# Kernel optimization log

Hardware: AMD Instinct MI355X
Metric: run time of the kernel (lower is better)

## Reference

```python
import jax, jax.numpy as jnp
import numpy as np

C = 512
C8 = C // 8  # 64
B, L = 32, 1024


def setup_inputs() -> dict:
    key = jax.random.key(0)
    ks = jax.random.split(key, 8)
    s = 0.05
    return {
        "x": jax.random.normal(ks[0], (B, C, L), dtype=jnp.float32),
        "Wq": jax.random.normal(ks[1], (C8, C), dtype=jnp.float32) * s,
        "bq": jax.random.normal(ks[2], (C8,), dtype=jnp.float32) * s,
        "Wk": jax.random.normal(ks[3], (C8, C), dtype=jnp.float32) * s,
        "bk": jax.random.normal(ks[4], (C8,), dtype=jnp.float32) * s,
        "Wv": jax.random.normal(ks[5], (C, C), dtype=jnp.float32) * s,
        "bv": jax.random.normal(ks[6], (C,), dtype=jnp.float32) * s,
        "gamma": jax.random.normal(ks[7], (1,), dtype=jnp.float32) * s,
    }


def reference(x, Wq, bq, Wk, bk, Wv, bv, gamma):
    # kernel-size-1 Conv1d == per-position matmul over channels
    q = jnp.einsum('dc,bcl->bdl', Wq, x) + bq[None, :, None]  # [B, C8, L]
    k = jnp.einsum('dc,bcl->bdl', Wk, x) + bk[None, :, None]  # [B, C8, L]
    v = jnp.einsum('oc,bcl->bol', Wv, x) + bv[None, :, None]  # [B, C, L]
    # energy[b, l, m] = <q[:, l], k[:, m]>  (no 1/sqrt(d) scaling, as in source)
    energy = jnp.einsum('bdl,bdm->blm', q, k)                 # [B, L, L]
    attention = jax.nn.softmax(energy, axis=-1)               # softmax over m
    # out[b, c, l] = sum_m v[b, c, m] * attention[b, l, m]
    out = jnp.einsum('bcm,blm->bcl', v, attention)            # [B, C, L]
    out = gamma[0] * out + x
    return (out, attention)
```

## Files before the change

kernel.cpp:

```cpp
#include <hip/hip_runtime.h>

typedef __attribute__((ext_vector_type(8))) short short8;
typedef __attribute__((ext_vector_type(4))) float f32x4;

#define B_SZ 32
#define C_IN 512
#define C8V 64
#define LSEQ 1024
#define OUT_ELEMS (B_SZ * C_IN * LSEQ)

__device__ inline unsigned short bf16_rn(float f) {
  unsigned int u = __float_as_uint(f);
  unsigned int r = 0x7FFFu + ((u >> 16) & 1u);
  return (unsigned short)((u + r) >> 16);
}
__device__ inline float bf16_to_f32(unsigned short h) {
  return __uint_as_float(((unsigned int)h) << 16);
}
__device__ inline void split_bf16(float f, unsigned short &hi, unsigned short &lo) {
  hi = bf16_rn(f);
  lo = bf16_rn(f - bf16_to_f32(hi));
}

__global__ __launch_bounds__(256) void split_weights(
    const float* __restrict__ Wq, const float* __restrict__ Wk, const float* __restrict__ Wv,
    unsigned short* __restrict__ Wqh, unsigned short* __restrict__ Wql,
    unsigned short* __restrict__ Wkh, unsigned short* __restrict__ Wkl,
    unsigned short* __restrict__ Wvh)
{
  int i = (blockIdx.x * 256 + threadIdx.x) * 4;
  if (i < 262144) {
    f32x4 f = *(const f32x4*)&Wv[i];
    #pragma unroll
    for (int j = 0; j < 4; ++j) Wvh[i + j] = bf16_rn(f[j]);
  } else if (i < 294912) {
    int k = i - 262144;
    f32x4 f = *(const f32x4*)&Wq[k];
    #pragma unroll
    for (int j = 0; j < 4; ++j) { unsigned short h, l; split_bf16(f[j], h, l); Wqh[k+j] = h; Wql[k+j] = l; }
  } else {
    int k = i - 294912;
    f32x4 f = *(const f32x4*)&Wk[k];
    #pragma unroll
    for (int j = 0; j < 4; ++j) { unsigned short h, l; split_bf16(f[j], h, l); Wkh[k+j] = h; Wkl[k+j] = l; }
  }
}

__global__ __launch_bounds__(256, 2) void qk_proj(
    const float* __restrict__ x,
    const unsigned short* __restrict__ Wqh, const unsigned short* __restrict__ Wql,
    const unsigned short* __restrict__ Wkh, const unsigned short* __restrict__ Wkl,
    const float* __restrict__ bq, const float* __restrict__ bk,
    unsigned short* __restrict__ qh, unsigned short* __restrict__ ql,
    unsigned short* __restrict__ kh, unsigned short* __restrict__ kl)
{
  const int nt = blockIdx.x;
  const int b  = blockIdx.y;
  const int tid = threadIdx.x;
  const int wave = tid >> 6, lane = tid & 63;
  const int wr = wave >> 1, wc = wave & 1;
  const int g = lane >> 4, ln = lane & 15;

  __shared__ char smem[66560];
  unsigned short* Ah = (unsigned short*)smem;
  unsigned short* Al = Ah + 128*64;
  unsigned short* Bh = Al + 128*64;
  unsigned short* Bl = Bh + 64*64;
  float* xs = (float*)(Bl + 64*64);

  f32x4 acc[4][2] = {};

  for (int kb = 0; kb < 8; ++kb) {
    if (kb) __syncthreads();
    #pragma unroll
    for (int i = 0; i < 4; ++i) {
      int idx = tid + i*256;
      int r = idx >> 3, jj = idx & 7;
      const unsigned short* sH = (r < 64) ? &Wqh[r*512 + kb*64 + jj*8]
                                          : &Wkh[(r-64)*512 + kb*64 + jj*8];
      const unsigned short* sL = (r < 64) ? &Wql[r*512 + kb*64 + jj*8]
                                          : &Wkl[(r-64)*512 + kb*64 + jj*8];
      int dst = r*64 + ((jj ^ (r & 7)) << 3);
      *(short8*)&Ah[dst] = *(const short8*)sH;
      *(short8*)&Al[dst] = *(const short8*)sL;
    }
    #pragma unroll
    for (int i = 0; i < 4; ++i) {
      int idx = tid + i*256;
      int kk = idx >> 4, l4 = idx & 15;
      f32x4 v = *(const f32x4*)&x[((long)b*C_IN + kb*64 + kk)*LSEQ + nt*64 + l4*4];
      *(f32x4*)&xs[kk*68 + l4*4] = v;
    }
    __syncthreads();
    {
      int l = tid & 63, kc = (tid >> 6) * 16;
      unsigned short hbuf[16], lbuf[16];
      #pragma unroll
      for (int i = 0; i < 16; ++i) split_bf16(xs[(kc + i)*68 + l], hbuf[i], lbuf[i]);
      #pragma unroll
      for (int s2 = 0; s2 < 2; ++s2) {
        int s = (kc >> 3) + s2;
        int dst = l*64 + ((s ^ (l & 7)) << 3);
        *(short8*)&Bh[dst] = *(const short8*)&hbuf[s2*8];
        *(short8*)&Bl[dst] = *(const short8*)&lbuf[s2*8];
      }
    }
    __syncthreads();
    __builtin_amdgcn_s_setprio(1);
    #pragma unroll
    for (int ks = 0; ks < 2; ++ks) {
      short8 bhf[2], blf[2];
      #pragma unroll
      for (int ni = 0; ni < 2; ++ni) {
        int cr = wc*32 + ni*16 + ln;
        int s = ((ks*4 + g) ^ (cr & 7)) << 3;
        bhf[ni] = *(const short8*)&Bh[cr*64 + s];
        blf[ni] = *(const short8*)&Bl[cr*64 + s];
      }
      #pragma unroll
      for (int mi = 0; mi < 4; ++mi) {
        int ar = wr*64 + mi*16 + ln;
        int s = ((ks*4 + g) ^ (ar & 7)) << 3;
        short8 ahf = *(const short8*)&Ah[ar*64 + s];
        short8 alf = *(const short8*)&Al[ar*64 + s];
        #pragma unroll
        for (int ni = 0; ni < 2; ++ni) {
          acc[mi][ni] = __builtin_amdgcn_mfma_f32_16x16x32_bf16(ahf, bhf[ni], acc[mi][ni], 0,0,0);
          acc[mi][ni] = __builtin_amdgcn_mfma_f32_16x16x32_bf16(ahf, blf[ni], acc[mi][ni], 0,0,0);
          acc[mi][ni] = __builtin_amdgcn_mfma_f32_16x16x32_bf16(alf, bhf[ni], acc[mi][ni], 0,0,0);
        }
      }
    }
    __builtin_amdgcn_s_setprio(0);
  }
  __syncthreads();
  unsigned short* Trh = (unsigned short*)smem;
  unsigned short* Trl = Trh + 64*136;
  #pragma unroll
  for (int mi = 0; mi < 4; ++mi)
    #pragma unroll
    for (int ni = 0; ni < 2; ++ni)
      #pragma unroll
      for (int j = 0; j < 4; ++j) {
        int rloc = wr*64 + mi*16 + g*4 + j;
        int cloc = wc*32 + ni*16 + ln;
        float bias = (rloc < 64) ? bq[rloc] : bk[rloc - 64];
        unsigned short hi, lo; split_bf16(acc[mi][ni][j] + bias, hi, lo);
        Trh[cloc*136 + rloc] = hi;
        Trl[cloc*136 + rloc] = lo;
      }
  __syncthreads();
  #pragma unroll
  for (int i = 0; i < 4; ++i) {
    int idx = tid + i*256;
    int l = idx >> 4, s = idx & 15;
    long row = ((long)b*LSEQ + nt*64 + l) * 64;
    short8 h  = *(const short8*)&Trh[l*136 + s*8];
    short8 lo = *(const short8*)&Trl[l*136 + s*8];
    if (s < 8) { *(short8*)&qh[row + s*8] = h;      *(short8*)&ql[row + s*8] = lo; }
    else       { *(short8*)&kh[row + (s-8)*8] = h;  *(short8*)&kl[row + (s-8)*8] = lo; }
  }
}

__global__ __launch_bounds__(256, 2) void v_proj(
    const float* __restrict__ x,
    const unsigned short* __restrict__ Wvh,
    const float* __restrict__ bv,
    unsigned short* __restrict__ vws)
{
  const int gi = blockIdx.x;
  const int b  = (gi & 7) + 8 * (gi >> 8);
  const int t  = (gi >> 3) & 31;
  const int lt = t & 7, ct = t >> 3;
  const int tid = threadIdx.x;
  const int wave = tid >> 6, lane = tid & 63;
  const int wr = wave >> 1, wc = wave & 1;
  const int g = lane >> 4, ln = lane & 15;

  __shared__ char smem[66560];
  unsigned short* Ahs = (unsigned short*)smem;
  unsigned short* Bhs = Ahs + 8192;
  float* xs = (float*)(Bhs + 8192);

  f32x4 acc[4][4] = {};

  for (int kb = 0; kb < 8; ++kb) {
    if (kb) __syncthreads();
    #pragma unroll
    for (int i = 0; i < 4; ++i) {
      int idx = tid + i*256;
      int r = idx >> 3, jj = idx & 7;
      *(short8*)&Ahs[r*64 + ((jj ^ (r & 7)) << 3)] =
        *(const short8*)&Wvh[(ct*128 + r)*512 + kb*64 + jj*8];
    }
    #pragma unroll
    for (int i = 0; i < 8; ++i) {
      int idx = tid + i*256;
      int kk = idx >> 5, l4 = idx & 31;
      f32x4 v = *(const f32x4*)&x[((long)b*C_IN + kb*64 + kk)*LSEQ + lt*128 + l4*4];
      *(f32x4*)&xs[kk*132 + l4*4] = v;
    }
    __syncthreads();
    {
      int l = tid & 127, kc = (tid >> 7) * 32;
      unsigned short hbuf[32];
      #pragma unroll
      for (int i = 0; i < 32; ++i) hbuf[i] = bf16_rn(xs[(kc + i)*132 + l]);
      #pragma unroll
      for (int s2 = 0; s2 < 4; ++s2) {
        int s = (kc >> 3) + s2;
        *(short8*)&Bhs[l*64 + ((s ^ (l & 7)) << 3)] = *(const short8*)&hbuf[s2*8];
      }
    }
    __syncthreads();
    __builtin_amdgcn_s_setprio(1);
    #pragma unroll
    for (int ks = 0; ks < 2; ++ks) {
      short8 bf[4];
      #pragma unroll
      for (int ni = 0; ni < 4; ++ni) {
        int cr = wc*64 + ni*16 + ln;
        bf[ni] = *(const short8*)&Bhs[cr*64 + (((ks*4 + g) ^ (cr & 7)) << 3)];
      }
      #pragma unroll
      for (int mi = 0; mi < 4; ++mi) {
        int ar = wr*64 + mi*16 + ln;
        short8 af = *(const short8*)&Ahs[ar*64 + (((ks*4 + g) ^ (ar & 7)) << 3)];
        #pragma unroll
        for (int ni = 0; ni < 4; ++ni)
          acc[mi][ni] = __builtin_amdgcn_mfma_f32_16x16x32_bf16(af, bf[ni], acc[mi][ni], 0,0,0);
      }
    }
    __builtin_amdgcn_s_setprio(0);
  }
  __syncthreads();
  unsigned short* Tr = (unsigned short*)smem;
  #pragma unroll
  for (int mi = 0; mi < 4; ++mi)
    #pragma unroll
    for (int ni = 0; ni < 4; ++ni)
      #pragma unroll
      for (int j = 0; j < 4; ++j) {
        int rloc = wr*64 + mi*16 + g*4 + j;
        int cloc = wc*64 + ni*16 + ln;
        Tr[rloc*136 + cloc] = bf16_rn(acc[mi][ni][j] + bv[ct*128 + rloc]);
      }
  __syncthreads();
  #pragma unroll
  for (int i = 0; i < 8; ++i) {
    int idx = tid + i*256;
    int c = idx >> 4, s = idx & 15;
    *(short8*)&vws[((long)b*C_IN + ct*128 + c)*LSEQ + lt*128 + s*8] =
      *(const short8*)&Tr[c*136 + s*8];
  }
}

__global__ __launch_bounds__(256, 2) void energy_softmax(
    const unsigned short* __restrict__ qh, const unsigned short* __restrict__ ql,
    const unsigned short* __restrict__ kh, const unsigned short* __restrict__ kl,
    float* __restrict__ attn, unsigned short* __restrict__ pbuf)
{
  const int gi = blockIdx.x;
  const int b  = (gi & 7) + 8 * (gi >> 9);
  const int lt = (gi >> 3) & 63;
  const int tid = threadIdx.x;
  const int wave = tid >> 6, lane = tid & 63;
  const int g = lane >> 4, ln = lane & 15;

  __shared__ unsigned short Ksm[16640];
  __shared__ float redM[4][16];
  __shared__ float redS[4][16];
  unsigned short* Kh = Ksm;
  unsigned short* Kl = Ksm + 8192;

  short8 ah[2], al[2];
  {
    long qrow = ((long)b*LSEQ + lt*16 + ln) * 64;
    #pragma unroll
    for (int ks = 0; ks < 2; ++ks) {
      ah[ks] = *(const short8*)&qh[qrow + ks*32 + g*8];
      al[ks] = *(const short8*)&ql[qrow + ks*32 + g*8];
    }
  }

  const int rb = tid >> 3, jj = tid & 7;
  const int dst0 = rb*64 + ((jj ^ (rb & 7)) << 3);
  const long kbase = ((long)b*LSEQ + rb)*64 + jj*8;

  short8 rkh[4], rkl[4];
  #pragma unroll
  for (int j = 0; j < 4; ++j) {
    rkh[j] = *(const short8*)&kh[kbase + j*2048];
    rkl[j] = *(const short8*)&kl[kbase + j*2048];
  }

  f32x4 acc[8][2] = {};
  #pragma unroll
  for (int c = 0; c < 8; ++c) {
    __syncthreads();
    #pragma unroll
    for (int j = 0; j < 4; ++j) {
      *(short8*)&Kh[dst0 + j*2048] = rkh[j];
      *(short8*)&Kl[dst0 + j*2048] = rkl[j];
    }
    __syncthreads();
    if (c < 7) {
      #pragma unroll
      for (int j = 0; j < 4; ++j) {
        rkh[j] = *(const short8*)&kh[kbase + (long)(c+1)*8192 + j*2048];
        rkl[j] = *(const short8*)&kl[kbase + (long)(c+1)*8192 + j*2048];
      }
    }
    __builtin_amdgcn_s_setprio(1);
    #pragma unroll
    for (int fq = 0; fq < 2; ++fq) {
      int mloc = wave*32 + fq*16 + ln;
      #pragma unroll
      for (int ks = 0; ks < 2; ++ks) {
        int s = ((ks*4 + g) ^ (mloc & 7)) << 3;
        short8 bh = *(const short8*)&Kh[mloc*64 + s];
        short8 bl = *(const short8*)&Kl[mloc*64 + s];
        acc[c][fq] = __builtin_amdgcn_mfma_f32_16x16x32_bf16(ah[ks], bh, acc[c][fq], 0,0,0);
        acc[c][fq] = __builtin_amdgcn_mfma_f32_16x16x32_bf16(ah[ks], bl, acc[c][fq], 0,0,0);
        acc[c][fq] = __builtin_amdgcn_mfma_f32_16x16x32_bf16(al[ks], bh, acc[c][fq], 0,0,0);
      }
    }
    __builtin_amdgcn_s_setprio(0);
  }

  float mx[4];
  #pragma unroll
  for (int j = 0; j < 4; ++j) {
    float m = -1e30f;
    #pragma unroll
    for (int c = 0; c < 8; ++c)
      #pragma unroll
      for (int fq = 0; fq < 2; ++fq) m = fmaxf(m, acc[c][fq][j]);
    #pragma unroll
    for (int off = 1; off < 16; off <<= 1) m = fmaxf(m, __shfl_xor(m, off));
    mx[j] = m;
  }
  if (ln == 0) {
    #pragma unroll
    for (int j = 0; j < 4; ++j) redM[wave][g*4+j] = mx[j];
  }
  __syncthreads();
  #pragma unroll
  for (int j = 0; j < 4; ++j) {
    float m = redM[0][g*4+j];
    #pragma unroll
    for (int w = 1; w < 4; ++w) m = fmaxf(m, redM[w][g*4+j]);
    mx[j] = m;
  }
  float sm[4];
  #pragma unroll
  for (int j = 0; j < 4; ++j) {
    float s = 0.f;
    #pragma unroll
    for (int c = 0; c < 8; ++c)
      #pragma unroll
      for (int fq = 0; fq < 2; ++fq) {
        float p = __expf(acc[c][fq][j] - mx[j]);
        acc[c][fq][j] = p;
        s += p;
      }
    #pragma unroll
    for (int off = 1; off < 16; off <<= 1) s += __shfl_xor(s, off);
    sm[j] = s;
  }
  if (ln == 0) {
    #pragma unroll
    for (int j = 0; j < 4; ++j) redS[wave][g*4+j] = sm[j];
  }
  __syncthreads();
  #pragma unroll
  for (int j = 0; j < 4; ++j) {
    float s = redS[0][g*4+j];
    #pragma unroll
    for (int w = 1; w < 4; ++w) s += redS[w][g*4+j];
    sm[j] = 1.0f / s;
  }

  unsigned short* Pb = Ksm;
  __syncthreads();
  #pragma unroll
  for (int c = 0; c < 8; ++c)
    #pragma unroll
    for (int fq = 0; fq < 2; ++fq) {
      int m0 = c*128 + wave*32 + fq*16 + ln;
      #pragma unroll
      for (int j = 0; j < 4; ++j)
        Pb[(g*4+j)*1032 + m0] = bf16_rn(acc[c][fq][j] * sm[j]);
    }
  __syncthreads();
  #pragma unroll
  for (int u = 0; u < 8; ++u) {
    int cid = tid + u*256;
    int row = cid >> 7, col = (cid & 127) * 8;
    short8 v = *(const short8*)&Pb[row*1032 + col];
    long gro = ((long)b*LSEQ + lt*16 + row)*LSEQ + col;
    *(short8*)&pbuf[gro] = v;
    f32x4 f0, f1;
    #pragma unroll
    for (int i = 0; i < 4; ++i) {
      f0[i] = bf16_to_f32((unsigned short)v[i]);
      f1[i] = bf16_to_f32((unsigned short)v[i+4]);
    }
    *(f32x4*)&attn[gro] = f0;
    *(f32x4*)&attn[gro + 4] = f1;
  }
}

__global__ __launch_bounds__(512, 2) void pv_out(
    const unsigned short* __restrict__ vws,
    const unsigned short* __restrict__ pbuf,
    const float* __restrict__ x,
    const float* __restrict__ gamma,
    float* __restrict__ out)
{
  const int gi = blockIdx.x;
  const int b  = (gi & 7) + 8 * (gi >> 7);
  const int t  = (gi >> 3) & 15;
  const int lt = t >> 2, ct = t & 3;
  const int tid = threadIdx.x;
  const int w = tid >> 6, lane = tid & 63;
  const int wcq = w >> 2, wlq = w & 3;
  const int g = lane >> 4, ln = lane & 15;

  __shared__ char smem[49152];
  unsigned short* Vst = (unsigned short*)smem;
  unsigned short* Pst = (unsigned short*)(smem + 16384);

  const int vr = tid >> 2, vs0 = (tid & 3) * 2;
  const long vbase = ((long)b*C_IN + ct*128 + vr)*LSEQ + vs0*8;
  const int pr = tid >> 1, ps0 = (tid & 1) * 4;
  const long pbase = ((long)b*LSEQ + lt*256 + pr)*LSEQ + ps0*8;

  f32x4 acc[4][4] = {};
  short8 rv[2], rp[4];
  #pragma unroll
  for (int j = 0; j < 2; ++j) rv[j] = *(const short8*)&vws[vbase + j*8];
  #pragma unroll
  for (int j = 0; j < 4; ++j) rp[j] = *(const short8*)&pbuf[pbase + j*8];

  for (int mb = 0; mb < 16; ++mb) {
    __syncthreads();
    #pragma unroll
    for (int j = 0; j < 2; ++j)
      *(short8*)&Vst[vr*64 + (((vs0 + j) ^ (vr & 7)) << 3)] = rv[j];
    #pragma unroll
    for (int j = 0; j < 4; ++j)
      *(short8*)&Pst[pr*64 + (((ps0 + j) ^ (pr & 7)) << 3)] = rp[j];
    __syncthreads();
    if (mb < 15) {
      #pragma unroll
      for (int j = 0; j < 2; ++j) rv[j] = *(const short8*)&vws[vbase + (mb+1)*64 + j*8];
      #pragma unroll
      for (int j = 0; j < 4; ++j) rp[j] = *(const short8*)&pbuf[pbase + (mb+1)*64 + j*8];
    }
    __builtin_amdgcn_s_setprio(1);
    #pragma unroll
    for (int ks = 0; ks < 2; ++ks) {
      short8 bf[4];
      #pragma unroll
      for (int lf = 0; lf < 4; ++lf) {
        int prow = wlq*64 + lf*16 + ln;
        bf[lf] = *(const short8*)&Pst[prow*64 + (((ks*4 + g) ^ (prow & 7)) << 3)];
      }
      #pragma unroll
      for (int cf = 0; cf < 4; ++cf) {
        int cr = wcq*64 + cf*16 + ln;
        short8 af = *(const short8*)&Vst[cr*64 + (((ks*4 + g) ^ (cr & 7)) << 3)];
        #pragma unroll
        for (int lf = 0; lf < 4; ++lf)
          acc[cf][lf] = __builtin_amdgcn_mfma_f32_16x16x32_bf16(af, bf[lf], acc[cf][lf], 0,0,0);
      }
    }
    __builtin_amdgcn_s_setprio(0);
  }

  const float gm = gamma[0];
  #pragma unroll
  for (int cf = 0; cf < 4; ++cf)
    #pragma unroll
    for (int lf = 0; lf < 4; ++lf)
      #pragma unroll
      for (int j = 0; j < 4; ++j) {
        int c = ct*128 + wcq*64 + cf*16 + g*4 + j;
        int l = lt*256 + wlq*64 + lf*16 + ln;
        long o = ((long)b*C_IN + c)*LSEQ + l;
        out[o] = gm * acc[cf][lf][j] + x[o];
      }
}

extern "C" void kernel_launch(void* const* d_in, const int* in_sizes, int n_in,
                              void* d_out, int out_size, void* d_ws, size_t ws_size,
                              hipStream_t stream)
{
  const float* x  = (const float*)d_in[0];
  const float* Wq = (const float*)d_in[1];
  const float* bq = (const float*)d_in[2];
  const float* Wk = (const float*)d_in[3];
  const float* bk = (const float*)d_in[4];
  const float* Wv = (const float*)d_in[5];
  const float* bv = (const float*)d_in[6];
  const float* gamma = (const float*)d_in[7];
  float* out  = (float*)d_out;
  float* attn = out + OUT_ELEMS;

  char* ws = (char*)d_ws;
  unsigned short* Wqh = (unsigned short*)(ws + 0);
  unsigned short* Wql = (unsigned short*)(ws + 65536);
  unsigned short* Wkh = (unsigned short*)(ws + 131072);
  unsigned short* Wkl = (unsigned short*)(ws + 196608);
  unsigned short* Wvh = (unsigned short*)(ws + 262144);
  unsigned short* qhp = (unsigned short*)(ws + 786432);
  unsigned short* qlp = (unsigned short*)(ws + 786432 + 1ul*4194304);
  unsigned short* khp = (unsigned short*)(ws + 786432 + 2ul*4194304);
  unsigned short* klp = (unsigned short*)(ws + 786432 + 3ul*4194304);
  unsigned short* vws = (unsigned short*)(ws + 786432 + 4ul*4194304);
  unsigned short* pbuf = (unsigned short*)(ws + 786432 + 4ul*4194304 + 33554432);

  split_weights<<<320, 256, 0, stream>>>(Wq, Wk, Wv, Wqh, Wql, Wkh, Wkl, Wvh);
  qk_proj<<<dim3(16, B_SZ), 256, 0, stream>>>(x, Wqh, Wql, Wkh, Wkl, bq, bk, qhp, qlp, khp, klp);
  v_proj<<<1024, 256, 0, stream>>>(x, Wvh, bv, vws);
  energy_softmax<<<2048, 256, 0, stream>>>(qhp, qlp, khp, klp, attn, pbuf);
  pv_out<<<512, 512, 0, stream>>>(vws, pbuf, x, gamma, out);
}
```

Before: 190.5 us.

## Register-prefetch next K-tile in QK and V projections, drop fp32 x staging

The QK and V projection kernels now load the next K-block of weights and x into registers before running the current block's MFMAs, so global loads overlap with compute. The fp32 x staging buffer in shared memory is removed: each thread loads a column of x straight into registers and converts it to bf16. This cuts one barrier per iteration and shrinks LDS use, which may allow more blocks per CU. The costs are higher register pressure and scalar strided x loads in place of vector loads.

```diff
diff --git a/kernel.cpp b/kernel.cpp
--- a/kernel.cpp
+++ b/kernel.cpp
@@ -61,51 +61,65 @@
   const int wr = wave >> 1, wc = wave & 1;
   const int g = lane >> 4, ln = lane & 15;
 
-  __shared__ char smem[66560];
+  __shared__ char smem[49152];
   unsigned short* Ah = (unsigned short*)smem;
-  unsigned short* Al = Ah + 128*64;
-  unsigned short* Bh = Al + 128*64;
-  unsigned short* Bl = Bh + 64*64;
-  float* xs = (float*)(Bl + 64*64);
+  unsigned short* Al = Ah + 8192;
+  unsigned short* Bh = Al + 8192;
+  unsigned short* Bl = Bh + 4096;
+
+  const int rb = tid >> 3, jj = tid & 7;
+  const int adst0 = rb*64 + ((jj ^ (rb & 7)) << 3);
+  const int xl = tid & 63, xkg = (tid >> 6) * 16;
+  const int bdst0 = xl*64 + (((xkg >> 3) ^ (xl & 7)) << 3);
+  const long xcol = (long)b*C_IN*LSEQ + (long)nt*64 + xl;
+
+  short8 rAh[4], rAl[4];
+  float xv[16];
+  rAh[0] = *(const short8*)&Wqh[rb*C_IN + jj*8];
+  rAh[1] = *(const short8*)&Wqh[(rb+32)*C_IN + jj*8];
+  rAh[2] = *(const short8*)&Wkh[rb*C_IN + jj*8];
+  rAh[3] = *(const short8*)&Wkh[(rb+32)*C_IN + jj*8];
+  rAl[0] = *(const short8*)&Wql[rb*C_IN + jj*8];
+  rAl[1] = *(const short8*)&Wql[(rb+32)*C_IN + jj*8];
+  rAl[2] = *(const short8*)&Wkl[rb*C_IN + jj*8];
+  rAl[3] = *(const short8*)&Wkl[(rb+32)*C_IN + jj*8];
+  #pragma unroll
+  for (int i = 0; i < 16; ++i) xv[i] = x[xcol + (long)(xkg + i)*LSEQ];
 
   f32x4 acc[4][2] = {};
 
   for (int kb = 0; kb < 8; ++kb) {
-    if (kb) __syncthreads();
-    #pragma unroll
-    for (int i = 0; i < 4; ++i) {
-      int idx = tid + i*256;
-      int r = idx >> 3, jj = idx & 7;
-      const unsigned short* sH = (r < 64) ? &Wqh[r*512 + kb*64 + jj*8]
-                                          : &Wkh[(r-64)*512 + kb*64 + jj*8];
-      const unsigned short* sL = (r < 64) ? &Wql[r*512 + kb*64 + jj*8]
-                                          : &Wkl[(r-64)*512 + kb*64 + jj*8];
-      int dst = r*64 + ((jj ^ (r & 7)) << 3);
-      *(short8*)&Ah[dst] = *(const short8*)sH;
-      *(short8*)&Al[dst] = *(const short8*)sL;
-    }
-    #pragma unroll
-    for (int i = 0; i < 4; ++i) {
-      int idx = tid + i*256;
-      int kk = idx >> 4, l4 = idx & 15;
-      f32x4 v = *(const f32x4*)&x[((long)b*C_IN + kb*64 + kk)*LSEQ + nt*64 + l4*4];
-      *(f32x4*)&xs[kk*68 + l4*4] = v;
-    }
-    __syncthreads();
+    __syncthreads();
+    #pragma unroll
+    for (int j = 0; j < 4; ++j) {
+      *(short8*)&Ah[adst0 + j*2048] = rAh[j];
+      *(short8*)&Al[adst0 + j*2048] = rAl[j];
+    }
     {
-      int l = tid & 63, kc = (tid >> 6) * 16;
-      unsigned short hbuf[16], lbuf[16];
-      #pragma unroll
-      for (int i = 0; i < 16; ++i) split_bf16(xs[(kc + i)*68 + l], hbuf[i], lbuf[i]);
+      unsigned short hb[16], lb[16];
+      #pragma unroll
+      for (int i = 0; i < 16; ++i) split_bf16(xv[i], hb[i], lb[i]);
       #pragma unroll
       for (int s2 = 0; s2 < 2; ++s2) {
-        int s = (kc >> 3) + s2;
-        int dst = l*64 + ((s ^ (l & 7)) << 3);
-        *(short8*)&Bh[dst] = *(const short8*)&hbuf[s2*8];
-        *(short8*)&Bl[dst] = *(const short8*)&lbuf[s2*8];
-      }
-    }
-    __syncthreads();
+        int d = xl*64 + ((((xkg >> 3) + s2) ^ (xl & 7)) << 3);
+        *(short8*)&Bh[d] = *(const short8*)&hb[s2*8];
+        *(short8*)&Bl[d] = *(const short8*)&lb[s2*8];
+      }
+    }
+    __syncthreads();
+    if (kb < 7) {
+      int ko = (kb+1)*64;
+      rAh[0] = *(const short8*)&Wqh[rb*C_IN + ko + jj*8];
+      rAh[1] = *(const short8*)&Wqh[(rb+32)*C_IN + ko + jj*8];
+      rAh[2] = *(const short8*)&Wkh[rb*C_IN + ko + jj*8];
+      rAh[3] = *(const short8*)&Wkh[(rb+32)*C_IN + ko + jj*8];
+      rAl[0] = *(const short8*)&Wql[rb*C_IN + ko + jj*8];
+      rAl[1] = *(const short8*)&Wql[(rb+32)*C_IN + ko + jj*8];
+      rAl[2] = *(const short8*)&Wkl[rb*C_IN + ko + jj*8];
+      rAl[3] = *(const short8*)&Wkl[(rb+32)*C_IN + ko + jj*8];
+      #pragma unroll
+      for (int i = 0; i < 16; ++i) xv[i] = x[xcol + (long)(ko + xkg + i)*LSEQ];
+    }
     __builtin_amdgcn_s_setprio(1);
     #pragma unroll
     for (int ks = 0; ks < 2; ++ks) {
@@ -177,42 +191,48 @@
   const int wr = wave >> 1, wc = wave & 1;
   const int g = lane >> 4, ln = lane & 15;
 
-  __shared__ char smem[66560];
+  __shared__ char smem[34816];
   unsigned short* Ahs = (unsigned short*)smem;
   unsigned short* Bhs = Ahs + 8192;
-  float* xs = (float*)(Bhs + 8192);
+
+  const int rb = tid >> 3, jj = tid & 7;
+  const int adst0 = rb*64 + ((jj ^ (rb & 7)) << 3);
+  const long wbase = (long)(ct*128 + rb)*C_IN + jj*8;
+  const int xl = tid & 127, xkg = (tid >> 7) * 32;
+  const long xcol = (long)b*C_IN*LSEQ + (long)lt*128 + xl;
+
+  short8 rA[4];
+  float xv[32];
+  #pragma unroll
+  for (int j = 0; j < 4; ++j) rA[j] = *(const short8*)&Wvh[wbase + (long)j*32*C_IN];
+  #pragma unroll
+  for (int i = 0; i < 32; ++i) xv[i] = x[xcol + (long)(xkg + i)*LSEQ];
 
   f32x4 acc[4][4] = {};
 
   for (int kb = 0; kb < 8; ++kb) {
-    if (kb) __syncthreads();
-    #pragma unroll
-    for (int i = 0; i < 4; ++i) {
-      int idx = tid + i*256;
-      int r = idx >> 3, jj = idx & 7;
-      *(short8*)&Ahs[r*64 + ((jj ^ (r & 7)) << 3)] =
-        *(const short8*)&Wvh[(ct*128 + r)*512 + kb*64 + jj*8];
-    }
-    #pragma unroll
-    for (int i = 0; i < 8; ++i) {
-      int idx = tid + i*256;
-      int kk = idx >> 5, l4 = idx & 31;
-      f32x4 v = *(const f32x4*)&x[((long)b*C_IN + kb*64 + kk)*LSEQ + lt*128 + l4*4];
-      *(f32x4*)&xs[kk*132 + l4*4] = v;
-    }
-    __syncthreads();
+    __syncthreads();
+    #pragma unroll
+    for (int j = 0; j < 4; ++j)
+      *(short8*)&Ahs[adst0 + j*2048] = rA[j];
     {
-      int l = tid & 127, kc = (tid >> 7) * 32;
-      unsigned short hbuf[32];
-      #pragma unroll
-      for (int i = 0; i < 32; ++i) hbuf[i] = bf16_rn(xs[(kc + i)*132 + l]);
+      unsigned short hb[32];
+      #pragma unroll
+      for (int i = 0; i < 32; ++i) hb[i] = bf16_rn(xv[i]);
       #pragma unroll
       for (int s2 = 0; s2 < 4; ++s2) {
-        int s = (kc >> 3) + s2;
-        *(short8*)&Bhs[l*64 + ((s ^ (l & 7)) << 3)] = *(const short8*)&hbuf[s2*8];
-      }
-    }
-    __syncthreads();
+        int d = xl*64 + ((((xkg >> 3) + s2) ^ (xl & 7)) << 3);
+        *(short8*)&Bhs[d] = *(const short8*)&hb[s2*8];
+      }
+    }
+    __syncthreads();
+    if (kb < 7) {
+      int ko = (kb+1)*64;
+      #pragma unroll
+      for (int j = 0; j < 4; ++j) rA[j] = *(const short8*)&Wvh[wbase + (long)j*32*C_IN + ko];
+      #pragma unroll
+      for (int i = 0; i < 32; ++i) xv[i] = x[xcol + (long)(ko + xkg + i)*LSEQ];
+    }
     __builtin_amdgcn_s_setprio(1);
     #pragma unroll
     for (int ks = 0; ks < 2; ++ks) {
```

After: 183.6 us. -3.6%, faster.
